# Kernel tuning notes

Measured on AMD Instinct MI355X. Metric: run time of the kernel, lower is better.

The kernel has to match this reference:

```python
import jax, jax.numpy as jnp
import numpy as np

N = 50000
E = 800000
IN_C = 64
OUT_C = 64
K = 2
GATE_C = IN_C + OUT_C
LAMBDA_MAX = 2.0


def _lap_norm(edge_index, edge_weight, n):
    # PyG ChebConv norm: sym Laplacian L = I - D^-1/2 A D^-1/2, scaled 2L/lmax - I.
    # With lambda_max=2 the diagonal term is (2/lmax)*1 - 1 = 0, so only the
    # off-diagonal weights -(2/lmax) * w_norm remain.
    row, col = edge_index[0], edge_index[1]
    deg = jax.ops.segment_sum(edge_weight, row, num_segments=n)
    dinv = jnp.where(deg > 0, jax.lax.rsqrt(jnp.where(deg > 0, deg, 1.0)), 0.0)
    lw = -(2.0 / LAMBDA_MAX) * edge_weight * dinv[row] * dinv[col]
    diag = jnp.full((n,), 2.0 / LAMBDA_MAX - 1.0, edge_weight.dtype)  # zeros for lmax=2
    return row, col, lw, diag


def _cheb_conv(x, row, col, lw, diag, Ws, b):
    # Ws: [K, C_in, C_out]; Tx_0 = x, Tx_1 = L_hat x, Tx_k = 2 L_hat Tx_{k-1} - Tx_{k-2}
    n = x.shape[0]

    def prop(h):  # L_hat @ h  via edge gather/scatter + diagonal
        msg = lw[:, None] * h[col]                      # [E, C]
        return jax.ops.segment_sum(msg, row, num_segments=n) + diag[:, None] * h

    Tx0 = x
    out = Tx0 @ Ws[0]
    Tx1 = prop(x)
    out = out + Tx1 @ Ws[1]
    for k in range(2, K):
        Tx2 = 2.0 * prop(Tx1) - Tx0
        out = out + Tx2 @ Ws[k]
        Tx0, Tx1 = Tx1, Tx2
    return out + b


def setup_inputs() -> dict:
    key = jax.random.key(0)
    ks = jax.random.split(key, 10)
    scale = 1.0 / np.sqrt(GATE_C)
    x = jax.random.normal(ks[0], (N, IN_C), jnp.float32)
    edge_index = jax.random.randint(ks[1], (2, E), 0, N, jnp.int64)
    edge_weight = jax.random.uniform(ks[2], (E,), jnp.float32)
    hidden_state = jax.random.normal(ks[3], (N, OUT_C), jnp.float32)
    Wz = jax.random.normal(ks[4], (K, GATE_C, OUT_C), jnp.float32) * scale
    Wr = jax.random.normal(ks[5], (K, GATE_C, OUT_C), jnp.float32) * scale
    Wh = jax.random.normal(ks[6], (K, GATE_C, OUT_C), jnp.float32) * scale
    bz = jnp.zeros((OUT_C,), jnp.float32)
    br = jnp.zeros((OUT_C,), jnp.float32)
    bh = jnp.zeros((OUT_C,), jnp.float32)
    return {"x": x, "edge_index": edge_index, "edge_weight": edge_weight,
            "hidden_state": hidden_state, "Wz": Wz, "bz": bz,
            "Wr": Wr, "br": br, "Wh": Wh, "bh": bh}


def reference(x, edge_index, edge_weight, hidden_state, Wz, bz, Wr, br, Wh, bh):
    n = x.shape[0]
    row, col, lw, diag = _lap_norm(edge_index, edge_weight, n)
    gate_input = jnp.concatenate([x, hidden_state], axis=-1)          # [N, GATE_C]
    z = jax.nn.sigmoid(_cheb_conv(gate_input, row, col, lw, diag, Wz, bz))
    r = jax.nn.sigmoid(_cheb_conv(gate_input, row, col, lw, diag, Wr, br))
    cand_in = jnp.concatenate([x, r * hidden_state], axis=-1)
    h_tilde = jnp.tanh(_cheb_conv(cand_in, row, col, lw, diag, Wh, bh))
    return (1.0 - z) * hidden_state + z * h_tilde
```

## Files before the change

### kernel.cpp

```cpp
#include <hip/hip_runtime.h>
#include <cstdint>

#define N_NODES 50000
#define N_EDGES 800000
#define C 64
#define SLOTS 64
#define B_N 120
#define NB 417
#define PCAP 2560
#define STG_BLOCKS 126
#define STG_CHUNK 6350

typedef __attribute__((ext_vector_type(8))) short bf16x8;
typedef __attribute__((ext_vector_type(4))) float f32x4;
typedef __attribute__((ext_vector_type(2))) float f32x2;

static constexpr size_t OFF_GCUR = 0;
static constexpr size_t OFF_DINV = 512;
static constexpr size_t OFF_CNT  = 50688;
static constexpr size_t OFF_BZR  = 100864;
static constexpr size_t OFF_BH   = 117248;
static constexpr size_t OFF_CSR  = 125440;
static constexpr size_t OFF_XH8  = OFF_CSR + (size_t)N_NODES * 64;
static constexpr size_t OFF_XB   = OFF_XH8 + (size_t)N_NODES * C / 2;
static constexpr size_t OFF_HB   = OFF_XB + (size_t)N_NODES * C / 2;
static constexpr size_t OFF_PXB  = OFF_HB + (size_t)N_NODES * C / 2;
static constexpr size_t OFF_RHB  = OFF_PXB + (size_t)N_NODES * C / 2;
static constexpr size_t OFF_RHD8 = OFF_RHB + (size_t)N_NODES * C / 2;
static constexpr size_t OFF_STG  = OFF_PXB;

__device__ __forceinline__ short f2bf(float f) {
    unsigned u = __float_as_uint(f);
    u += 0x7fffu + ((u >> 16) & 1u);
    return (short)(u >> 16);
}
__device__ __forceinline__ float bf_lo(unsigned v) { return __uint_as_float(v << 16); }
__device__ __forceinline__ float bf_hi(unsigned v) { return __uint_as_float(v & 0xffff0000u); }
__device__ __forceinline__ float bfu(unsigned short v) { return __uint_as_float((unsigned)v << 16); }
__device__ __forceinline__ float fast_sigmoid(float v) { return 1.f / (1.f + __expf(-v)); }
__device__ __forceinline__ float fast_tanh(float v) { return 1.f - 2.f / (__expf(2.f * v) + 1.f); }
__device__ __forceinline__ unsigned sel4u(unsigned a, unsigned b, unsigned c,
                                          unsigned d, int g) {
    unsigned r = (g & 1) ? b : a;
    unsigned s = (g & 1) ? d : c;
    return (g & 2) ? s : r;
}

#if defined(__has_builtin)
#if __has_builtin(__builtin_amdgcn_cvt_pk_f32_fp8) && __has_builtin(__builtin_amdgcn_cvt_pk_fp8_f32)
#define HW_FP8 1
#endif
#endif

#ifndef HW_FP8
__device__ __forceinline__ float fp8_dec1(unsigned b) {
    unsigned s = b >> 7, e = (b >> 3) & 15u, m = b & 7u;
    float v = e ? __uint_as_float(((e + 120u) << 23) | (m << 20))
                : (float)m * 0.001953125f;
    return s ? -v : v;
}
__device__ __forceinline__ unsigned fp8_enc1(float f) {
    float a = fabsf(f);
    unsigned s = (__float_as_uint(f) >> 31) << 7;
    if (!(a < 448.f)) return s | 0x7e;
    int msub = (int)rintf(a * 512.f);
    if (msub <= 7) return s | (unsigned)msub;
    int e; float fr = frexpf(a, &e);
    int mm = (int)rintf(fr * 16.f);
    if (mm == 16) { mm = 8; e += 1; }
    int se = e - 1 + 7;
    if (se >= 16) return s | 0x7e;
    return s | (unsigned)(se << 3) | (unsigned)(mm - 8);
}
#endif

template <int HI>
__device__ __forceinline__ f32x2 fp8x2_dec(unsigned u) {
#ifdef HW_FP8
    return __builtin_amdgcn_cvt_pk_f32_fp8(u, HI != 0);
#else
    f32x2 r;
    r[0] = fp8_dec1((u >> (HI * 16)) & 0xffu);
    r[1] = fp8_dec1((u >> (HI * 16 + 8)) & 0xffu);
    return r;
#endif
}
__device__ __forceinline__ unsigned fp8x2_enc(float a, float b) {
#ifdef HW_FP8
    return (unsigned)__builtin_amdgcn_cvt_pk_fp8_f32(a, b, 0, false) & 0xffffu;
#else
    return fp8_enc1(a) | (fp8_enc1(b) << 8);
#endif
}

__global__ __launch_bounds__(256) void zero_pack_kernel(
        int* __restrict__ gcur,
        const float* __restrict__ Wz, const float* __restrict__ Wr,
        const float* __restrict__ Wh,
        short* __restrict__ Bzr, short* __restrict__ Bh) {
    if (blockIdx.x == 24) {
        gcur[threadIdx.x] = 0;
        gcur[256 + threadIdx.x] = 0;
        return;
    }
    int gid = blockIdx.x * 256 + threadIdx.x;
    if (gid < 4096) {
        int ktct = gid >> 6, lane = gid & 63;
        int kt = ktct >> 3, ct = ktct & 7;
        int colg = ct * 16 + (lane & 15);
        int k0 = kt * 32 + (lane >> 4) * 8;
        const float* W = (colg < 64) ? Wz : Wr;
        int c = colg & 63;
        short v[8];
        #pragma unroll
        for (int j = 0; j < 8; ++j) {
            int k = k0 + j;
            v[j] = f2bf(W[(k >> 7) * (128 * 64) + (k & 127) * 64 + c]);
        }
        *(bf16x8*)(Bzr + (size_t)ktct * 512 + lane * 8) = *(bf16x8*)v;
    } else {
        int idx = gid - 4096;
        int ktct = idx >> 6, lane = idx & 63;
        int kt = ktct >> 2, ct = ktct & 3;
        int colg = ct * 16 + (lane & 15);
        int k0 = kt * 32 + (lane >> 4) * 8;
        short v[8];
        #pragma unroll
        for (int j = 0; j < 8; ++j) {
            int k = k0 + j;
            v[j] = f2bf(Wh[(k >> 7) * (128 * 64) + (k & 127) * 64 + colg]);
        }
        *(bf16x8*)(Bh + (size_t)ktct * 512 + lane * 8) = *(bf16x8*)v;
    }
}

__global__ __launch_bounds__(512) void stage_kernel(
        const int* __restrict__ row, const int* __restrict__ col,
        const float* __restrict__ w,
        int* __restrict__ gcur, uint2* __restrict__ stg) {
    __shared__ int lcnt[NB];
    __shared__ int lbase[NB];
    int tid = threadIdx.x;
    int e0 = blockIdx.x * STG_CHUNK;
    int e1 = min(e0 + STG_CHUNK, N_EDGES);
    for (int i = tid; i < NB; i += 512) lcnt[i] = 0;
    __syncthreads();
    for (int e = e0 + tid; e < e1; e += 512)
        atomicAdd(&lcnt[row[e] / B_N], 1);
    __syncthreads();
    for (int i = tid; i < NB; i += 512) {
        int c = lcnt[i];
        lbase[i] = c ? atomicAdd(&gcur[i], c) : 0;
        lcnt[i] = 0;
    }
    __syncthreads();
    for (int e = e0 + tid; e < e1; e += 512) {
        int r = row[e];
        int b = r / B_N;
        int off = atomicAdd(&lcnt[b], 1);
        int pos = lbase[b] + off;
        unsigned cw = ((unsigned)col[e] << 16) | (unsigned short)f2bf(w[e]);
        if (pos < PCAP)
            stg[(size_t)b * PCAP + pos] = make_uint2((unsigned)(r - b * B_N), cw);
    }
}

__global__ __launch_bounds__(256) void sort_kernel(
        const int* __restrict__ gcur, const uint2* __restrict__ stg,
        const float* __restrict__ x, const float* __restrict__ h,
        unsigned* __restrict__ csr, int* __restrict__ cnt, float* __restrict__ dinv,
        unsigned* __restrict__ xh8,
        unsigned short* __restrict__ xb, unsigned short* __restrict__ hb) {
    __shared__ int lcnt[B_N];
    __shared__ int lbase[B_N];
    __shared__ float ldeg[B_N];
    __shared__ float ldv[B_N];
    __shared__ int scanb[128];
    __shared__ unsigned lbuf[PCAP];
    __shared__ unsigned char lnode[PCAP];
    int b = blockIdx.x, tid = threadIdx.x;
    int n0 = b * B_N;
    int m = min(gcur[b], PCAP);
    for (int i = tid; i < B_N; i += 256) { lcnt[i] = 0; ldeg[i] = 0.f; }
    __syncthreads();
    const uint2* s = stg + (size_t)b * PCAP;
    for (int i = tid; i < m; i += 256) {
        uint2 e = s[i];
        atomicAdd(&lcnt[e.x], 1);
        atomicAdd(&ldeg[e.x], bf_lo(e.y));
    }
    __syncthreads();
    if (tid < 128) scanb[tid] = (tid < B_N) ? lcnt[tid] : 0;
    __syncthreads();
    for (int d = 1; d < 128; d <<= 1) {
        int v = 0;
        if (tid < 128 && tid >= d) v = scanb[tid - d];
        __syncthreads();
        if (tid < 128) scanb[tid] += v;
        __syncthreads();
    }
    if (tid < B_N) { lbase[tid] = scanb[tid] - lcnt[tid]; lcnt[tid] = 0; }
    __syncthreads();
    for (int i = tid; i < m; i += 256) {
        uint2 e = s[i];
        int off = atomicAdd(&lcnt[e.x], 1);
        int p = lbase[e.x] + off;
        lbuf[p] = e.y;
        lnode[p] = (unsigned char)e.x;
    }
    __syncthreads();
    for (int i = tid; i < m; i += 256) {
        int nl = lnode[i];
        int pos = i - lbase[nl];
        csr[(size_t)(n0 + nl) * SLOTS + pos] = lbuf[i];
    }
    for (int i = tid; i < B_N * 8; i += 256) {
        int nl = i >> 3;
        int node = n0 + nl;
        if (node >= N_NODES) continue;
        int mm = min(lcnt[nl], SLOTS);
        int pe = (mm + 7) & ~7;
        if (pe == 0) pe = 8;
        int idx = mm + (i & 7);
        if (idx < pe) csr[(size_t)node * SLOTS + idx] = 0u;
    }
    if (tid < B_N) {
        int node = n0 + tid;
        if (node < N_NODES) {
            cnt[node] = lcnt[tid];
            float d = ldeg[tid];
            float dv = (d > 0.f) ? rsqrtf(d) : 0.f;
            dinv[node] = dv;
            ldv[tid] = dv;
        } else ldv[tid] = 0.f;
    }
    __syncthreads();
    for (int i = tid; i < B_N * 16; i += 256) {
        int g = n0 * 16 + i;
        if (g >= N_NODES * 16) continue;
        float dv = ldv[i >> 4];
        float4 xv = ((const float4*)x)[g];
        float4 hv = ((const float4*)h)[g];
        unsigned p01 = fp8x2_enc(xv.x * dv, hv.x * dv) |
                       (fp8x2_enc(xv.y * dv, hv.y * dv) << 16);
        unsigned p23 = fp8x2_enc(xv.z * dv, hv.z * dv) |
                       (fp8x2_enc(xv.w * dv, hv.w * dv) << 16);
        ((uint2*)xh8)[g] = make_uint2(p01, p23);
        ((short4*)xb)[g] = make_short4(f2bf(xv.x), f2bf(xv.y), f2bf(xv.z), f2bf(xv.w));
        ((short4*)hb)[g] = make_short4(f2bf(hv.x), f2bf(hv.y), f2bf(hv.z), f2bf(hv.w));
    }
}

__global__ __launch_bounds__(256) void prop_gemm_zr_kernel(
        const int* __restrict__ cnt, const unsigned* __restrict__ csr,
        const float* __restrict__ dinv, const unsigned* __restrict__ xh8,
        const unsigned short* __restrict__ xb, const unsigned short* __restrict__ hb,
        const short* __restrict__ Bzr,
        const float* __restrict__ bz, const float* __restrict__ br,
        unsigned short* __restrict__ Pxb,
        float* __restrict__ z, unsigned short* __restrict__ rhb,
        unsigned char* __restrict__ rhd8) {
    __shared__ __align__(16) unsigned short lpx[16][72];
    __shared__ __align__(16) unsigned short lph[16][72];
    int tid = threadIdx.x;
    int wid = __builtin_amdgcn_readfirstlane(tid >> 6);
    int lane = tid & 63;
    int lane15 = lane & 15;
    int g4 = lane >> 4;
    int node0 = blockIdx.x * 16;

    #pragma unroll
    for (int i = 0; i < 2; ++i) {
        int nlA = wid * 4 + i * 2;
        int nA = node0 + nlA;
        int2 cc = *(const int2*)(cnt + nA);
        int gqA = (min(cc.x, SLOTS) + 7) >> 3;
        int gqB = (min(cc.y, SLOTS) + 7) >> 3;
        const uint4* sA = (const uint4*)(csr + (size_t)nA * SLOTS);
        const uint4* sB = (const uint4*)(csr + (size_t)(nA + 1) * SLOTS);
        f32x4 axA = {0.f,0.f,0.f,0.f}, ahA = {0.f,0.f,0.f,0.f};
        f32x4 axB = {0.f,0.f,0.f,0.f}, ahB = {0.f,0.f,0.f,0.f};
        int gmax = max(gqA, gqB);
        for (int g = 0; g < gmax; ++g) {
            bool doA = g < gqA, doB = g < gqB;
            uint4 a0, a1, b0, b1;
            uint2 vA0, vA1, vB0, vB1;
            unsigned eA0, eA1, eB0, eB1;
            if (doA) { a0 = sA[2 * g]; a1 = sA[2 * g + 1]; }
            if (doB) { b0 = sB[2 * g]; b1 = sB[2 * g + 1]; }
            if (doA) {
                eA0 = sel4u(a0.x, a0.y, a0.z, a0.w, g4);
                eA1 = sel4u(a1.x, a1.y, a1.z, a1.w, g4);
                vA0 = *(const uint2*)(xh8 + (size_t)(eA0 >> 16) * 32 + lane15 * 2);
                vA1 = *(const uint2*)(xh8 + (size_t)(eA1 >> 16) * 32 + lane15 * 2);
            }
            if (doB) {
                eB0 = sel4u(b0.x, b0.y, b0.z, b0.w, g4);
                eB1 = sel4u(b1.x, b1.y, b1.z, b1.w, g4);
                vB0 = *(const uint2*)(xh8 + (size_t)(eB0 >> 16) * 32 + lane15 * 2);
                vB1 = *(const uint2*)(xh8 + (size_t)(eB1 >> 16) * 32 + lane15 * 2);
            }
            if (doA) {
                float w0 = bf_lo(eA0), w1 = bf_lo(eA1);
                f32x2 p;
                p = fp8x2_dec<0>(vA0.x); axA[0] = fmaf(w0, p[0], axA[0]); ahA[0] = fmaf(w0, p[1], ahA[0]);
                p = fp8x2_dec<1>(vA0.x); axA[1] = fmaf(w0, p[0], axA[1]); ahA[1] = fmaf(w0, p[1], ahA[1]);
                p = fp8x2_dec<0>(vA0.y); axA[2] = fmaf(w0, p[0], axA[2]); ahA[2] = fmaf(w0, p[1], ahA[2]);
                p = fp8x2_dec<1>(vA0.y); axA[3] = fmaf(w0, p[0], axA[3]); ahA[3] = fmaf(w0, p[1], ahA[3]);
                p = fp8x2_dec<0>(vA1.x); axA[0] = fmaf(w1, p[0], axA[0]); ahA[0] = fmaf(w1, p[1], ahA[0]);
                p = fp8x2_dec<1>(vA1.x); axA[1] = fmaf(w1, p[0], axA[1]); ahA[1] = fmaf(w1, p[1], ahA[1]);
                p = fp8x2_dec<0>(vA1.y); axA[2] = fmaf(w1, p[0], axA[2]); ahA[2] = fmaf(w1, p[1], ahA[2]);
                p = fp8x2_dec<1>(vA1.y); axA[3] = fmaf(w1, p[0], axA[3]); ahA[3] = fmaf(w1, p[1], ahA[3]);
            }
            if (doB) {
                float w0 = bf_lo(eB0), w1 = bf_lo(eB1);
                f32x2 p;
                p = fp8x2_dec<0>(vB0.x); axB[0] = fmaf(w0, p[0], axB[0]); ahB[0] = fmaf(w0, p[1], ahB[0]);
                p = fp8x2_dec<1>(vB0.x); axB[1] = fmaf(w0, p[0], axB[1]); ahB[1] = fmaf(w0, p[1], ahB[1]);
                p = fp8x2_dec<0>(vB0.y); axB[2] = fmaf(w0, p[0], axB[2]); ahB[2] = fmaf(w0, p[1], ahB[2]);
                p = fp8x2_dec<1>(vB0.y); axB[3] = fmaf(w0, p[0], axB[3]); ahB[3] = fmaf(w0, p[1], ahB[3]);
                p = fp8x2_dec<0>(vB1.x); axB[0] = fmaf(w1, p[0], axB[0]); ahB[0] = fmaf(w1, p[1], ahB[0]);
                p = fp8x2_dec<1>(vB1.x); axB[1] = fmaf(w1, p[0], axB[1]); ahB[1] = fmaf(w1, p[1], ahB[1]);
                p = fp8x2_dec<0>(vB1.y); axB[2] = fmaf(w1, p[0], axB[2]); ahB[2] = fmaf(w1, p[1], ahB[2]);
                p = fp8x2_dec<1>(vB1.y); axB[3] = fmaf(w1, p[0], axB[3]); ahB[3] = fmaf(w1, p[1], ahB[3]);
            }
        }
        #pragma unroll
        for (int j = 0; j < 4; ++j) {
            axA[j] += __shfl_xor(axA[j], 16, 64); axA[j] += __shfl_xor(axA[j], 32, 64);
            ahA[j] += __shfl_xor(ahA[j], 16, 64); ahA[j] += __shfl_xor(ahA[j], 32, 64);
            axB[j] += __shfl_xor(axB[j], 16, 64); axB[j] += __shfl_xor(axB[j], 32, 64);
            ahB[j] += __shfl_xor(ahB[j], 16, 64); ahB[j] += __shfl_xor(ahB[j], 32, 64);
        }
        float2 dvp = *(const float2*)(dinv + nA);
        if (g4 == 0) {
            float sA1 = -dvp.x, sB1 = -dvp.y;
            short4 pxA = make_short4(f2bf(sA1 * axA[0]), f2bf(sA1 * axA[1]),
                                     f2bf(sA1 * axA[2]), f2bf(sA1 * axA[3]));
            short4 phA = make_short4(f2bf(sA1 * ahA[0]), f2bf(sA1 * ahA[1]),
                                     f2bf(sA1 * ahA[2]), f2bf(sA1 * ahA[3]));
            short4 pxB = make_short4(f2bf(sB1 * axB[0]), f2bf(sB1 * axB[1]),
                                     f2bf(sB1 * axB[2]), f2bf(sB1 * axB[3]));
            short4 phB = make_short4(f2bf(sB1 * ahB[0]), f2bf(sB1 * ahB[1]),
                                     f2bf(sB1 * ahB[2]), f2bf(sB1 * ahB[3]));
            *(short4*)(&lpx[nlA][lane15 * 4]) = pxA;
            *(short4*)(&lph[nlA][lane15 * 4]) = phA;
            *(short4*)(&lpx[nlA + 1][lane15 * 4]) = pxB;
            *(short4*)(&lph[nlA + 1][lane15 * 4]) = phB;
            *(short4*)(Pxb + (size_t)nA * C + lane15 * 4) = pxA;
            *(short4*)(Pxb + (size_t)(nA + 1) * C + lane15 * 4) = pxB;
        }
    }
    __syncthreads();

    int q = lane >> 4;
    int nl = lane & 15;
    f32x4 acc[2];
    acc[0] = (f32x4){0.f, 0.f, 0.f, 0.f};
    acc[1] = (f32x4){0.f, 0.f, 0.f, 0.f};
    const bf16x8* Bp = (const bf16x8*)Bzr;
    #pragma unroll
    for (int kt = 0; kt < 8; ++kt) {
        bf16x8 a;
        if (kt < 4) {
            const unsigned short* src = (kt < 2) ? xb : hb;
            a = *(const bf16x8*)(src + (size_t)(node0 + nl) * C + (kt & 1) * 32 + q * 8);
        } else {
            const unsigned short* src = (kt < 6) ? &lpx[0][0] : &lph[0][0];
            a = *(const bf16x8*)(src + nl * 72 + (kt & 1) * 32 + q * 8);
        }
        #pragma unroll
        for (int c2 = 0; c2 < 2; ++c2) {
            int ct = wid * 2 + c2;
            bf16x8 bfr = Bp[(kt * 8 + ct) * 64 + lane];
            acc[c2] = __builtin_amdgcn_mfma_f32_16x16x32_bf16(a, bfr, acc[c2], 0, 0, 0);
        }
    }

    if (wid < 2) {
        #pragma unroll
        for (int c2 = 0; c2 < 2; ++c2) {
            int colg = (wid * 2 + c2) * 16 + nl;
            float bias = bz[colg];
            #pragma unroll
            for (int r = 0; r < 4; ++r) {
                int node = node0 + q * 4 + r;
                z[(size_t)node * C + colg] = fast_sigmoid(acc[c2][r] + bias);
            }
        }
    } else {
        float dv[4];
        #pragma unroll
        for (int r = 0; r < 4; ++r) dv[r] = dinv[node0 + q * 4 + r];
        #pragma unroll
        for (int c2 = 0; c2 < 2; ++c2) {
            int oc = (wid * 2 + c2 - 4) * 16 + nl;
            float bias = br[oc];
            #pragma unroll
            for (int r = 0; r < 4; ++r) {
                int node = node0 + q * 4 + r;
                float sg = fast_sigmoid(acc[c2][r] + bias);
                float rhv = sg * bfu(hb[(size_t)node * C + oc]);
                rhb[(size_t)node * C + oc] = (unsigned short)f2bf(rhv);
                rhd8[(size_t)node * C + oc] =
                    (unsigned char)(fp8x2_enc(rhv * dv[r], 0.f) & 0xffu);
            }
        }
    }
}

__global__ __launch_bounds__(256) void prop_gemm_h_kernel(
        const int* __restrict__ cnt, const unsigned* __restrict__ csr,
        const float* __restrict__ dinv, const unsigned* __restrict__ rhd8,
        const unsigned short* __restrict__ xb, const unsigned short* __restrict__ rhb,
        const unsigned short* __restrict__ Pxb,
        const short* __restrict__ Bh, const float* __restrict__ bh,
        const float* __restrict__ z, const float* __restrict__ h,
        float* __restrict__ out) {
    __shared__ __align__(16) unsigned short lpr[16][72];
    int tid = threadIdx.x;
    int wid = __builtin_amdgcn_readfirstlane(tid >> 6);
    int lane = tid & 63;
    int lane15 = lane & 15;
    int g4 = lane >> 4;
    int node0 = blockIdx.x * 16;

    #pragma unroll
    for (int i = 0; i < 2; ++i) {
        int nlA = wid * 4 + i * 2;
        int nA = node0 + nlA;
        int2 cc = *(const int2*)(cnt + nA);
        int gqA = (min(cc.x, SLOTS) + 7) >> 3;
        int gqB = (min(cc.y, SLOTS) + 7) >> 3;
        const uint4* sA = (const uint4*)(csr + (size_t)nA * SLOTS);
        const uint4* sB = (const uint4*)(csr + (size_t)(nA + 1) * SLOTS);
        f32x4 aA = {0.f,0.f,0.f,0.f}, aB = {0.f,0.f,0.f,0.f};
        int gmax = max(gqA, gqB);
        for (int g = 0; g < gmax; ++g) {
            bool doA = g < gqA, doB = g < gqB;
            uint4 a0, a1, b0, b1;
            unsigned vA0, vA1, vB0, vB1;
            unsigned eA0, eA1, eB0, eB1;
            if (doA) { a0 = sA[2 * g]; a1 = sA[2 * g + 1]; }
            if (doB) { b0 = sB[2 * g]; b1 = sB[2 * g + 1]; }
            if (doA) {
                eA0 = sel4u(a0.x, a0.y, a0.z, a0.w, g4);
                eA1 = sel4u(a1.x, a1.y, a1.z, a1.w, g4);
                vA0 = rhd8[(size_t)(eA0 >> 16) * 16 + lane15];
                vA1 = rhd8[(size_t)(eA1 >> 16) * 16 + lane15];
            }
            if (doB) {
                eB0 = sel4u(b0.x, b0.y, b0.z, b0.w, g4);
                eB1 = sel4u(b1.x, b1.y, b1.z, b1.w, g4);
                vB0 = rhd8[(size_t)(eB0 >> 16) * 16 + lane15];
                vB1 = rhd8[(size_t)(eB1 >> 16) * 16 + lane15];
            }
            if (doA) {
                float w0 = bf_lo(eA0), w1 = bf_lo(eA1);
                f32x2 p;
                p = fp8x2_dec<0>(vA0); aA[0] = fmaf(w0, p[0], aA[0]); aA[1] = fmaf(w0, p[1], aA[1]);
                p = fp8x2_dec<1>(vA0); aA[2] = fmaf(w0, p[0], aA[2]); aA[3] = fmaf(w0, p[1], aA[3]);
                p = fp8x2_dec<0>(vA1); aA[0] = fmaf(w1, p[0], aA[0]); aA[1] = fmaf(w1, p[1], aA[1]);
                p = fp8x2_dec<1>(vA1); aA[2] = fmaf(w1, p[0], aA[2]); aA[3] = fmaf(w1, p[1], aA[3]);
            }
            if (doB) {
                float w0 = bf_lo(eB0), w1 = bf_lo(eB1);
                f32x2 p;
                p = fp8x2_dec<0>(vB0); aB[0] = fmaf(w0, p[0], aB[0]); aB[1] = fmaf(w0, p[1], aB[1]);
                p = fp8x2_dec<1>(vB0); aB[2] = fmaf(w0, p[0], aB[2]); aB[3] = fmaf(w0, p[1], aB[3]);
                p = fp8x2_dec<0>(vB1); aB[0] = fmaf(w1, p[0], aB[0]); aB[1] = fmaf(w1, p[1], aB[1]);
                p = fp8x2_dec<1>(vB1); aB[2] = fmaf(w1, p[0], aB[2]); aB[3] = fmaf(w1, p[1], aB[3]);
            }
        }
        #pragma unroll
        for (int j = 0; j < 4; ++j) {
            aA[j] += __shfl_xor(aA[j], 16, 64); aA[j] += __shfl_xor(aA[j], 32, 64);
            aB[j] += __shfl_xor(aB[j], 16, 64); aB[j] += __shfl_xor(aB[j], 32, 64);
        }
        float2 dvp = *(const float2*)(dinv + nA);
        if (g4 == 0) {
            float sA1 = -dvp.x, sB1 = -dvp.y;
            short4 prA = make_short4(f2bf(sA1 * aA[0]), f2bf(sA1 * aA[1]),
                                     f2bf(sA1 * aA[2]), f2bf(sA1 * aA[3]));
            short4 prB = make_short4(f2bf(sB1 * aB[0]), f2bf(sB1 * aB[1]),
                                     f2bf(sB1 * aB[2]), f2bf(sB1 * aB[3]));
            *(short4*)(&lpr[nlA][lane15 * 4]) = prA;
            *(short4*)(&lpr[nlA + 1][lane15 * 4]) = prB;
        }
    }
    __syncthreads();

    int q = lane >> 4;
    int nl = lane & 15;
    f32x4 acc = (f32x4){0.f, 0.f, 0.f, 0.f};
    const bf16x8* Bp = (const bf16x8*)Bh;
    #pragma unroll
    for (int kt = 0; kt < 8; ++kt) {
        bf16x8 a;
        if (kt < 6) {
            const unsigned short* src = (kt < 2) ? xb : (kt < 4) ? rhb : Pxb;
            a = *(const bf16x8*)(src + (size_t)(node0 + nl) * C + (kt & 1) * 32 + q * 8);
        } else {
            a = *(const bf16x8*)(&lpr[0][0] + nl * 72 + (kt & 1) * 32 + q * 8);
        }
        bf16x8 bfr = Bp[(kt * 4 + wid) * 64 + lane];
        acc = __builtin_amdgcn_mfma_f32_16x16x32_bf16(a, bfr, acc, 0, 0, 0);
    }

    int oc = wid * 16 + nl;
    float bias = bh[oc];
    #pragma unroll
    for (int r = 0; r < 4; ++r) {
        int node = node0 + q * 4 + r;
        float ht = fast_tanh(acc[r] + bias);
        float zz = z[(size_t)node * C + oc];
        float hv = h[(size_t)node * C + oc];
        out[(size_t)node * C + oc] = (1.f - zz) * hv + zz * ht;
    }
}

extern "C" void kernel_launch(void* const* d_in, const int* in_sizes, int n_in,
                              void* d_out, int out_size, void* d_ws, size_t ws_size,
                              hipStream_t stream) {
    const float* x    = (const float*)d_in[0];
    const int*   eidx = (const int*)  d_in[1];
    const float* w    = (const float*)d_in[2];
    const float* h    = (const float*)d_in[3];
    const float* Wz   = (const float*)d_in[4];
    const float* bz   = (const float*)d_in[5];
    const float* Wr   = (const float*)d_in[6];
    const float* br   = (const float*)d_in[7];
    const float* Wh   = (const float*)d_in[8];
    const float* bh   = (const float*)d_in[9];
    float* out = (float*)d_out;
    float* ws  = (float*)d_ws;

    const int* row = eidx;
    const int* col = eidx + N_EDGES;

    int*            gcur = (int*)(ws + OFF_GCUR);
    float*          dinv = ws + OFF_DINV;
    int*            cnt  = (int*)(ws + OFF_CNT);
    unsigned*       csr  = (unsigned*)(ws + OFF_CSR);
    short*          Bzr  = (short*)(ws + OFF_BZR);
    short*          Bh   = (short*)(ws + OFF_BH);
    unsigned*       xh8  = (unsigned*)(ws + OFF_XH8);
    unsigned short* xb   = (unsigned short*)(ws + OFF_XB);
    unsigned short* hb   = (unsigned short*)(ws + OFF_HB);
    unsigned short* Pxb  = (unsigned short*)(ws + OFF_PXB);
    unsigned short* rhb  = (unsigned short*)(ws + OFF_RHB);
    unsigned char*  rhd8 = (unsigned char*)(ws + OFF_RHD8);
    uint2*          stg  = (uint2*)(ws + OFF_STG);
    float*          z    = out;

    zero_pack_kernel<<<25, 256, 0, stream>>>(gcur, Wz, Wr, Wh, Bzr, Bh);

    stage_kernel<<<STG_BLOCKS, 512, 0, stream>>>(row, col, w, gcur, stg);

    sort_kernel<<<NB, 256, 0, stream>>>(gcur, stg, x, h, csr, cnt, dinv, xh8, xb, hb);

    prop_gemm_zr_kernel<<<N_NODES / 16, 256, 0, stream>>>(
        cnt, csr, dinv, xh8, xb, hb, Bzr, bz, br, Pxb, z, rhb, rhd8);

    prop_gemm_h_kernel<<<N_NODES / 16, 256, 0, stream>>>(
        cnt, csr, dinv, (const unsigned*)rhd8, xb, rhb, Pxb, Bh, bh, z, h, out);
}
```

Baseline: 197.5 us.

## Fold weight packing into sort kernel, double stage blocks, packed f32x2 FMAs

Moves the bf16 weight packing out of the zero kernel into 12 extra blocks of the sort kernel, leaving a one-block zero kernel, so packing overlaps with sorting. It doubles the stage grid with half-size chunks and raises sort to 512 threads per block. The gather-accumulate loops in both prop kernels are rewritten with f32x2 vector multiply-adds so the compiler can emit packed FMAs. Larger sort blocks use the same shared memory but may lower occupancy, and more stage blocks add global atomics on the bucket counters.

```diff
diff --git a/kernel.cpp b/kernel.cpp
--- a/kernel.cpp
+++ b/kernel.cpp
@@ -8,8 +8,8 @@
 #define B_N 120
 #define NB 417
 #define PCAP 2560
-#define STG_BLOCKS 126
-#define STG_CHUNK 6350
+#define STG_BLOCKS 252
+#define STG_CHUNK 3175
 
 typedef __attribute__((ext_vector_type(8))) short bf16x8;
 typedef __attribute__((ext_vector_type(4))) float f32x4;
@@ -93,45 +93,9 @@
 #endif
 }
 
-__global__ __launch_bounds__(256) void zero_pack_kernel(
-        int* __restrict__ gcur,
-        const float* __restrict__ Wz, const float* __restrict__ Wr,
-        const float* __restrict__ Wh,
-        short* __restrict__ Bzr, short* __restrict__ Bh) {
-    if (blockIdx.x == 24) {
-        gcur[threadIdx.x] = 0;
-        gcur[256 + threadIdx.x] = 0;
-        return;
-    }
-    int gid = blockIdx.x * 256 + threadIdx.x;
-    if (gid < 4096) {
-        int ktct = gid >> 6, lane = gid & 63;
-        int kt = ktct >> 3, ct = ktct & 7;
-        int colg = ct * 16 + (lane & 15);
-        int k0 = kt * 32 + (lane >> 4) * 8;
-        const float* W = (colg < 64) ? Wz : Wr;
-        int c = colg & 63;
-        short v[8];
-        #pragma unroll
-        for (int j = 0; j < 8; ++j) {
-            int k = k0 + j;
-            v[j] = f2bf(W[(k >> 7) * (128 * 64) + (k & 127) * 64 + c]);
-        }
-        *(bf16x8*)(Bzr + (size_t)ktct * 512 + lane * 8) = *(bf16x8*)v;
-    } else {
-        int idx = gid - 4096;
-        int ktct = idx >> 6, lane = idx & 63;
-        int kt = ktct >> 2, ct = ktct & 3;
-        int colg = ct * 16 + (lane & 15);
-        int k0 = kt * 32 + (lane >> 4) * 8;
-        short v[8];
-        #pragma unroll
-        for (int j = 0; j < 8; ++j) {
-            int k = k0 + j;
-            v[j] = f2bf(Wh[(k >> 7) * (128 * 64) + (k & 127) * 64 + colg]);
-        }
-        *(bf16x8*)(Bh + (size_t)ktct * 512 + lane * 8) = *(bf16x8*)v;
-    }
+__global__ __launch_bounds__(256) void zero_kernel(int* __restrict__ gcur) {
+    gcur[threadIdx.x] = 0;
+    gcur[256 + threadIdx.x] = 0;
 }
 
 __global__ __launch_bounds__(512) void stage_kernel(
@@ -165,12 +129,49 @@
     }
 }
 
-__global__ __launch_bounds__(256) void sort_kernel(
+__global__ __launch_bounds__(512) void sort_kernel(
         const int* __restrict__ gcur, const uint2* __restrict__ stg,
         const float* __restrict__ x, const float* __restrict__ h,
         unsigned* __restrict__ csr, int* __restrict__ cnt, float* __restrict__ dinv,
         unsigned* __restrict__ xh8,
-        unsigned short* __restrict__ xb, unsigned short* __restrict__ hb) {
+        unsigned short* __restrict__ xb, unsigned short* __restrict__ hb,
+        const float* __restrict__ Wz, const float* __restrict__ Wr,
+        const float* __restrict__ Wh,
+        short* __restrict__ Bzr, short* __restrict__ Bh) {
+    int b = blockIdx.x, tid = threadIdx.x;
+    if (b >= NB) {
+        int gid = (b - NB) * 512 + tid;
+        if (gid < 4096) {
+            int ktct = gid >> 6, lane = gid & 63;
+            int kt = ktct >> 3, ct = ktct & 7;
+            int colg = ct * 16 + (lane & 15);
+            int k0 = kt * 32 + (lane >> 4) * 8;
+            const float* W = (colg < 64) ? Wz : Wr;
+            int c = colg & 63;
+            short v[8];
+            #pragma unroll
+            for (int j = 0; j < 8; ++j) {
+                int k = k0 + j;
+                v[j] = f2bf(W[(k >> 7) * (128 * 64) + (k & 127) * 64 + c]);
+            }
+            *(bf16x8*)(Bzr + (size_t)ktct * 512 + lane * 8) = *(bf16x8*)v;
+        } else {
+            int idx = gid - 4096;
+            int ktct = idx >> 6, lane = idx & 63;
+            int kt = ktct >> 2, ct = ktct & 3;
+            int colg = ct * 16 + (lane & 15);
+            int k0 = kt * 32 + (lane >> 4) * 8;
+            short v[8];
+            #pragma unroll
+            for (int j = 0; j < 8; ++j) {
+                int k = k0 + j;
+                v[j] = f2bf(Wh[(k >> 7) * (128 * 64) + (k & 127) * 64 + colg]);
+            }
+            *(bf16x8*)(Bh + (size_t)ktct * 512 + lane * 8) = *(bf16x8*)v;
+        }
+        return;
+    }
+
     __shared__ int lcnt[B_N];
     __shared__ int lbase[B_N];
     __shared__ float ldeg[B_N];
@@ -178,13 +179,12 @@
     __shared__ int scanb[128];
     __shared__ unsigned lbuf[PCAP];
     __shared__ unsigned char lnode[PCAP];
-    int b = blockIdx.x, tid = threadIdx.x;
     int n0 = b * B_N;
     int m = min(gcur[b], PCAP);
-    for (int i = tid; i < B_N; i += 256) { lcnt[i] = 0; ldeg[i] = 0.f; }
+    for (int i = tid; i < B_N; i += 512) { lcnt[i] = 0; ldeg[i] = 0.f; }
     __syncthreads();
     const uint2* s = stg + (size_t)b * PCAP;
-    for (int i = tid; i < m; i += 256) {
+    for (int i = tid; i < m; i += 512) {
         uint2 e = s[i];
         atomicAdd(&lcnt[e.x], 1);
         atomicAdd(&ldeg[e.x], bf_lo(e.y));
@@ -201,7 +201,7 @@
     }
     if (tid < B_N) { lbase[tid] = scanb[tid] - lcnt[tid]; lcnt[tid] = 0; }
     __syncthreads();
-    for (int i = tid; i < m; i += 256) {
+    for (int i = tid; i < m; i += 512) {
         uint2 e = s[i];
         int off = atomicAdd(&lcnt[e.x], 1);
         int p = lbase[e.x] + off;
@@ -209,12 +209,12 @@
         lnode[p] = (unsigned char)e.x;
     }
     __syncthreads();
-    for (int i = tid; i < m; i += 256) {
+    for (int i = tid; i < m; i += 512) {
         int nl = lnode[i];
         int pos = i - lbase[nl];
         csr[(size_t)(n0 + nl) * SLOTS + pos] = lbuf[i];
     }
-    for (int i = tid; i < B_N * 8; i += 256) {
+    for (int i = tid; i < B_N * 8; i += 512) {
         int nl = i >> 3;
         int node = n0 + nl;
         if (node >= N_NODES) continue;
@@ -235,7 +235,7 @@
         } else ldv[tid] = 0.f;
     }
     __syncthreads();
-    for (int i = tid; i < B_N * 16; i += 256) {
+    for (int i = tid; i < B_N * 16; i += 512) {
         int g = n0 * 16 + i;
         if (g >= N_NODES * 16) continue;
         float dv = ldv[i >> 4];
@@ -278,8 +278,8 @@
         int gqB = (min(cc.y, SLOTS) + 7) >> 3;
         const uint4* sA = (const uint4*)(csr + (size_t)nA * SLOTS);
         const uint4* sB = (const uint4*)(csr + (size_t)(nA + 1) * SLOTS);
-        f32x4 axA = {0.f,0.f,0.f,0.f}, ahA = {0.f,0.f,0.f,0.f};
-        f32x4 axB = {0.f,0.f,0.f,0.f}, ahB = {0.f,0.f,0.f,0.f};
+        f32x2 pA[4] = {{0.f,0.f},{0.f,0.f},{0.f,0.f},{0.f,0.f}};
+        f32x2 pB[4] = {{0.f,0.f},{0.f,0.f},{0.f,0.f},{0.f,0.f}};
         int gmax = max(gqA, gqB);
         for (int g = 0; g < gmax; ++g) {
             bool doA = g < gqA, doB = g < gqB;
@@ -302,47 +302,47 @@
             }
             if (doA) {
                 float w0 = bf_lo(eA0), w1 = bf_lo(eA1);
-                f32x2 p;
-                p = fp8x2_dec<0>(vA0.x); axA[0] = fmaf(w0, p[0], axA[0]); ahA[0] = fmaf(w0, p[1], ahA[0]);
-                p = fp8x2_dec<1>(vA0.x); axA[1] = fmaf(w0, p[0], axA[1]); ahA[1] = fmaf(w0, p[1], ahA[1]);
-                p = fp8x2_dec<0>(vA0.y); axA[2] = fmaf(w0, p[0], axA[2]); ahA[2] = fmaf(w0, p[1], ahA[2]);
-                p = fp8x2_dec<1>(vA0.y); axA[3] = fmaf(w0, p[0], axA[3]); ahA[3] = fmaf(w0, p[1], ahA[3]);
-                p = fp8x2_dec<0>(vA1.x); axA[0] = fmaf(w1, p[0], axA[0]); ahA[0] = fmaf(w1, p[1], ahA[0]);
-                p = fp8x2_dec<1>(vA1.x); axA[1] = fmaf(w1, p[0], axA[1]); ahA[1] = fmaf(w1, p[1], ahA[1]);
-                p = fp8x2_dec<0>(vA1.y); axA[2] = fmaf(w1, p[0], axA[2]); ahA[2] = fmaf(w1, p[1], ahA[2]);
-                p = fp8x2_dec<1>(vA1.y); axA[3] = fmaf(w1, p[0], axA[3]); ahA[3] = fmaf(w1, p[1], ahA[3]);
+                f32x2 w0v = {w0, w0}, w1v = {w1, w1};
+                pA[0] += w0v * fp8x2_dec<0>(vA0.x);
+                pA[1] += w0v * fp8x2_dec<1>(vA0.x);
+                pA[2] += w0v * fp8x2_dec<0>(vA0.y);
+                pA[3] += w0v * fp8x2_dec<1>(vA0.y);
+                pA[0] += w1v * fp8x2_dec<0>(vA1.x);
+                pA[1] += w1v * fp8x2_dec<1>(vA1.x);
+                pA[2] += w1v * fp8x2_dec<0>(vA1.y);
+                pA[3] += w1v * fp8x2_dec<1>(vA1.y);
             }
             if (doB) {
                 float w0 = bf_lo(eB0), w1 = bf_lo(eB1);
-                f32x2 p;
-                p = fp8x2_dec<0>(vB0.x); axB[0] = fmaf(w0, p[0], axB[0]); ahB[0] = fmaf(w0, p[1], ahB[0]);
-                p = fp8x2_dec<1>(vB0.x); axB[1] = fmaf(w0, p[0], axB[1]); ahB[1] = fmaf(w0, p[1], ahB[1]);
-                p = fp8x2_dec<0>(vB0.y); axB[2] = fmaf(w0, p[0], axB[2]); ahB[2] = fmaf(w0, p[1], ahB[2]);
-                p = fp8x2_dec<1>(vB0.y); axB[3] = fmaf(w0, p[0], axB[3]); ahB[3] = fmaf(w0, p[1], ahB[3]);
-                p = fp8x2_dec<0>(vB1.x); axB[0] = fmaf(w1, p[0], axB[0]); ahB[0] = fmaf(w1, p[1], ahB[0]);
-                p = fp8x2_dec<1>(vB1.x); axB[1] = fmaf(w1, p[0], axB[1]); ahB[1] = fmaf(w1, p[1], ahB[1]);
-                p = fp8x2_dec<0>(vB1.y); axB[2] = fmaf(w1, p[0], axB[2]); ahB[2] = fmaf(w1, p[1], ahB[2]);
-                p = fp8x2_dec<1>(vB1.y); axB[3] = fmaf(w1, p[0], axB[3]); ahB[3] = fmaf(w1, p[1], ahB[3]);
+                f32x2 w0v = {w0, w0}, w1v = {w1, w1};
+                pB[0] += w0v * fp8x2_dec<0>(vB0.x);
+                pB[1] += w0v * fp8x2_dec<1>(vB0.x);
+                pB[2] += w0v * fp8x2_dec<0>(vB0.y);
+                pB[3] += w0v * fp8x2_dec<1>(vB0.y);
+                pB[0] += w1v * fp8x2_dec<0>(vB1.x);
+                pB[1] += w1v * fp8x2_dec<1>(vB1.x);
+                pB[2] += w1v * fp8x2_dec<0>(vB1.y);
+                pB[3] += w1v * fp8x2_dec<1>(vB1.y);
             }
         }
         #pragma unroll
         for (int j = 0; j < 4; ++j) {
-            axA[j] += __shfl_xor(axA[j], 16, 64); axA[j] += __shfl_xor(axA[j], 32, 64);
-            ahA[j] += __shfl_xor(ahA[j], 16, 64); ahA[j] += __shfl_xor(ahA[j], 32, 64);
-            axB[j] += __shfl_xor(axB[j], 16, 64); axB[j] += __shfl_xor(axB[j], 32, 64);
-            ahB[j] += __shfl_xor(ahB[j], 16, 64); ahB[j] += __shfl_xor(ahB[j], 32, 64);
+            pA[j][0] += __shfl_xor(pA[j][0], 16, 64); pA[j][0] += __shfl_xor(pA[j][0], 32, 64);
+            pA[j][1] += __shfl_xor(pA[j][1], 16, 64); pA[j][1] += __shfl_xor(pA[j][1], 32, 64);
+            pB[j][0] += __shfl_xor(pB[j][0], 16, 64); pB[j][0] += __shfl_xor(pB[j][0], 32, 64);
+            pB[j][1] += __shfl_xor(pB[j][1], 16, 64); pB[j][1] += __shfl_xor(pB[j][1], 32, 64);
         }
         float2 dvp = *(const float2*)(dinv + nA);
         if (g4 == 0) {
             float sA1 = -dvp.x, sB1 = -dvp.y;
-            short4 pxA = make_short4(f2bf(sA1 * axA[0]), f2bf(sA1 * axA[1]),
-                                     f2bf(sA1 * axA[2]), f2bf(sA1 * axA[3]));
-            short4 phA = make_short4(f2bf(sA1 * ahA[0]), f2bf(sA1 * ahA[1]),
-                                     f2bf(sA1 * ahA[2]), f2bf(sA1 * ahA[3]));
-            short4 pxB = make_short4(f2bf(sB1 * axB[0]), f2bf(sB1 * axB[1]),
-                                     f2bf(sB1 * axB[2]), f2bf(sB1 * axB[3]));
-            short4 phB = make_short4(f2bf(sB1 * ahB[0]), f2bf(sB1 * ahB[1]),
-                                     f2bf(sB1 * ahB[2]), f2bf(sB1 * ahB[3]));
+            short4 pxA = make_short4(f2bf(sA1 * pA[0][0]), f2bf(sA1 * pA[1][0]),
+                                     f2bf(sA1 * pA[2][0]), f2bf(sA1 * pA[3][0]));
+            short4 phA = make_short4(f2bf(sA1 * pA[0][1]), f2bf(sA1 * pA[1][1]),
+                                     f2bf(sA1 * pA[2][1]), f2bf(sA1 * pA[3][1]));
+            short4 pxB = make_short4(f2bf(sB1 * pB[0][0]), f2bf(sB1 * pB[1][0]),
+                                     f2bf(sB1 * pB[2][0]), f2bf(sB1 * pB[3][0]));
+            short4 phB = make_short4(f2bf(sB1 * pB[0][1]), f2bf(sB1 * pB[1][1]),
+                                     f2bf(sB1 * pB[2][1]), f2bf(sB1 * pB[3][1]));
             *(short4*)(&lpx[nlA][lane15 * 4]) = pxA;
             *(short4*)(&lph[nlA][lane15 * 4]) = phA;
             *(short4*)(&lpx[nlA + 1][lane15 * 4]) = pxB;
@@ -434,7 +434,8 @@
         int gqB = (min(cc.y, SLOTS) + 7) >> 3;
         const uint4* sA = (const uint4*)(csr + (size_t)nA * SLOTS);
         const uint4* sB = (const uint4*)(csr + (size_t)(nA + 1) * SLOTS);
-        f32x4 aA = {0.f,0.f,0.f,0.f}, aB = {0.f,0.f,0.f,0.f};
+        f32x2 pA[2] = {{0.f,0.f},{0.f,0.f}};
+        f32x2 pB[2] = {{0.f,0.f},{0.f,0.f}};
         int gmax = max(gqA, gqB);
         for (int g = 0; g < gmax; ++g) {
             bool doA = g < gqA, doB = g < gqB;
@@ -457,33 +458,35 @@
             }
             if (doA) {
                 float w0 = bf_lo(eA0), w1 = bf_lo(eA1);
-                f32x2 p;
-                p = fp8x2_dec<0>(vA0); aA[0] = fmaf(w0, p[0], aA[0]); aA[1] = fmaf(w0, p[1], aA[1]);
-                p = fp8x2_dec<1>(vA0); aA[2] = fmaf(w0, p[0], aA[2]); aA[3] = fmaf(w0, p[1], aA[3]);
-                p = fp8x2_dec<0>(vA1); aA[0] = fmaf(w1, p[0], aA[0]); aA[1] = fmaf(w1, p[1], aA[1]);
-                p = fp8x2_dec<1>(vA1); aA[2] = fmaf(w1, p[0], aA[2]); aA[3] = fmaf(w1, p[1], aA[3]);
+                f32x2 w0v = {w0, w0}, w1v = {w1, w1};
+                pA[0] += w0v * fp8x2_dec<0>(vA0);
+                pA[1] += w0v * fp8x2_dec<1>(vA0);
+                pA[0] += w1v * fp8x2_dec<0>(vA1);
+                pA[1] += w1v * fp8x2_dec<1>(vA1);
             }
             if (doB) {
                 float w0 = bf_lo(eB0), w1 = bf_lo(eB1);
-                f32x2 p;
-                p = fp8x2_dec<0>(vB0); aB[0] = fmaf(w0, p[0], aB[0]); aB[1] = fmaf(w0, p[1], aB[1]);
-                p = fp8x2_dec<1>(vB0); aB[2] = fmaf(w0, p[0], aB[2]); aB[3] = fmaf(w0, p[1], aB[3]);
-                p = fp8x2_dec<0>(vB1); aB[0] = fmaf(w1, p[0], aB[0]); aB[1] = fmaf(w1, p[1], aB[1]);
-                p = fp8x2_dec<1>(vB1); aB[2] = fmaf(w1, p[0], aB[2]); aB[3] = fmaf(w1, p[1], aB[3]);
+                f32x2 w0v = {w0, w0}, w1v = {w1, w1};
+                pB[0] += w0v * fp8x2_dec<0>(vB0);
+                pB[1] += w0v * fp8x2_dec<1>(vB0);
+                pB[0] += w1v * fp8x2_dec<0>(vB1);
+                pB[1] += w1v * fp8x2_dec<1>(vB1);
             }
         }
         #pragma unroll
-        for (int j = 0; j < 4; ++j) {
-            aA[j] += __shfl_xor(aA[j], 16, 64); aA[j] += __shfl_xor(aA[j], 32, 64);
-            aB[j] += __shfl_xor(aB[j], 16, 64); aB[j] += __shfl_xor(aB[j], 32, 64);
+        for (int j = 0; j < 2; ++j) {
+            pA[j][0] += __shfl_xor(pA[j][0], 16, 64); pA[j][0] += __shfl_xor(pA[j][0], 32, 64);
+            pA[j][1] += __shfl_xor(pA[j][1], 16, 64); pA[j][1] += __shfl_xor(pA[j][1], 32, 64);
+            pB[j][0] += __shfl_xor(pB[j][0], 16, 64); pB[j][0] += __shfl_xor(pB[j][0], 32, 64);
+            pB[j][1] += __shfl_xor(pB[j][1], 16, 64); pB[j][1] += __shfl_xor(pB[j][1], 32, 64);
         }
         float2 dvp = *(const float2*)(dinv + nA);
         if (g4 == 0) {
             float sA1 = -dvp.x, sB1 = -dvp.y;
-            short4 prA = make_short4(f2bf(sA1 * aA[0]), f2bf(sA1 * aA[1]),
-                                     f2bf(sA1 * aA[2]), f2bf(sA1 * aA[3]));
-            short4 prB = make_short4(f2bf(sB1 * aB[0]), f2bf(sB1 * aB[1]),
-                                     f2bf(sB1 * aB[2]), f2bf(sB1 * aB[3]));
+            short4 prA = make_short4(f2bf(sA1 * pA[0][0]), f2bf(sA1 * pA[0][1]),
+                                     f2bf(sA1 * pA[1][0]), f2bf(sA1 * pA[1][1]));
+            short4 prB = make_short4(f2bf(sB1 * pB[0][0]), f2bf(sB1 * pB[0][1]),
+                                     f2bf(sB1 * pB[1][0]), f2bf(sB1 * pB[1][1]));
             *(short4*)(&lpr[nlA][lane15 * 4]) = prA;
             *(short4*)(&lpr[nlA + 1][lane15 * 4]) = prB;
         }
@@ -553,11 +556,12 @@
     uint2*          stg  = (uint2*)(ws + OFF_STG);
     float*          z    = out;
 
-    zero_pack_kernel<<<25, 256, 0, stream>>>(gcur, Wz, Wr, Wh, Bzr, Bh);
+    zero_kernel<<<1, 256, 0, stream>>>(gcur);
 
     stage_kernel<<<STG_BLOCKS, 512, 0, stream>>>(row, col, w, gcur, stg);
 
-    sort_kernel<<<NB, 256, 0, stream>>>(gcur, stg, x, h, csr, cnt, dinv, xh8, xb, hb);
+    sort_kernel<<<NB + 12, 512, 0, stream>>>(gcur, stg, x, h, csr, cnt, dinv,
+                                             xh8, xb, hb, Wz, Wr, Wh, Bzr, Bh);
 
     prop_gemm_zr_kernel<<<N_NODES / 16, 256, 0, stream>>>(
         cnt, csr, dinv, xh8, xb, hb, Bzr, bz, br, Pxb, z, rhb, rhd8);
```

After: 191.5 us (median of 2 runs). -3.1%, faster.
